# Optimization experiments

Measured on AMD Instinct MI355X. Metric: run time of the kernel, lower is better.

The kernel has to match this reference:

```python
import jax, jax.numpy as jnp
import numpy as np

D_MODEL = 512
N_HEADS = 8
D_HEAD = D_MODEL // N_HEADS
N_LAYERS = 6
VOCAB = 32000
B, S = 4, 1024
EPS = 1e-5


def positional_encoding(length, d_model):
    # matches get_positional_encoding_table: pos * (1/10000**(i/d)), sin on even i, cos on odd i
    inv = 1.0 / (10000.0 ** (jnp.arange(d_model, dtype=jnp.float32) / d_model))
    ang = jnp.arange(length, dtype=jnp.float32)[:, None] * inv[None, :]  # [S, D]
    pe = jnp.where(jnp.arange(d_model) % 2 == 0, jnp.sin(ang), jnp.cos(ang))
    return pe


def layer_norm(x, g, b):
    m = jnp.mean(x, axis=-1, keepdims=True)
    v = jnp.mean((x - m) ** 2, axis=-1, keepdims=True)
    return (x - m) * jax.lax.rsqrt(v + EPS) * g + b


def setup_inputs() -> dict:
    key = jax.random.key(0)
    ks = jax.random.split(key, 9)
    sc = 0.02
    return {
        "tokens": jax.random.randint(ks[0], (B, S), 0, VOCAB),
        "emb": jax.random.normal(ks[1], (VOCAB, D_MODEL), jnp.float32) * sc,
        "Wq": jax.random.normal(ks[2], (N_LAYERS, D_MODEL, D_MODEL), jnp.float32) * sc,
        "bq": jnp.zeros((N_LAYERS, D_MODEL), jnp.float32),
        "Wk": jax.random.normal(ks[3], (N_LAYERS, D_MODEL, D_MODEL), jnp.float32) * sc,
        "bk": jnp.zeros((N_LAYERS, D_MODEL), jnp.float32),
        "Wv": jax.random.normal(ks[4], (N_LAYERS, D_MODEL, D_MODEL), jnp.float32) * sc,
        "bv": jnp.zeros((N_LAYERS, D_MODEL), jnp.float32),
        "Wo": jax.random.normal(ks[5], (N_LAYERS, D_MODEL, D_MODEL), jnp.float32) * sc,
        "bo": jnp.zeros((N_LAYERS, D_MODEL), jnp.float32),
        "W1": jax.random.normal(ks[6], (N_LAYERS, D_MODEL, 4 * D_MODEL), jnp.float32) * sc,
        "b1": jnp.zeros((N_LAYERS, 4 * D_MODEL), jnp.float32),
        "W2": jax.random.normal(ks[7], (N_LAYERS, 4 * D_MODEL, D_MODEL), jnp.float32) * sc,
        "b2": jnp.zeros((N_LAYERS, D_MODEL), jnp.float32),
        "ln_g": jnp.ones((N_LAYERS, D_MODEL), jnp.float32),
        "ln_b": jnp.zeros((N_LAYERS, D_MODEL), jnp.float32),
    }


def encoder_layer(x, Wq, bq, Wk, bk, Wv, bv, Wo, bo, W1, b1, W2, b2, g, b):
    bsz = x.shape[0]
    q = (x @ Wq + bq).reshape(bsz, -1, N_HEADS, D_HEAD).transpose(0, 2, 1, 3)  # [B,h,S,dk]
    k = (x @ Wk + bk).reshape(bsz, -1, N_HEADS, D_HEAD).transpose(0, 2, 1, 3)
    v = (x @ Wv + bv).reshape(bsz, -1, N_HEADS, D_HEAD).transpose(0, 2, 1, 3)
    scores = jnp.einsum('bhqd,bhkd->bhqk', q, k) / (D_HEAD ** 0.5)
    w = jax.nn.softmax(scores, axis=-1)
    attn = jnp.einsum('bhqk,bhkd->bhqd', w, v)  # [B,h,S,dv]
    # faithful to source bug: .view(B,-1,h*dv) WITHOUT transposing heads back
    attn = attn.reshape(bsz, -1, N_HEADS * D_HEAD)  # [B,S,D] with heads/seq interleaved
    x = layer_norm(x + (attn @ Wo + bo), g, b)
    ffn = jnp.maximum(x @ W1 + b1, 0.0) @ W2 + b2
    x = layer_norm(x + ffn, g, b)  # same (shared) LayerNorm params, as in source
    return x


def reference(tokens, emb, Wq, bq, Wk, bk, Wv, bv, Wo, bo, W1, b1, W2, b2, ln_g, ln_b):
    x = emb[tokens]  # [B,S,D]
    x = x + positional_encoding(x.shape[1], D_MODEL)
    for i in range(N_LAYERS):
        x = encoder_layer(x, Wq[i], bq[i], Wk[i], bk[i], Wv[i], bv[i], Wo[i], bo[i],
                          W1[i], b1[i], W2[i], b2[i], ln_g[i], ln_b[i])
    return x
```

## Files before the change

kernel.cpp:

```cpp
#include <hip/hip_runtime.h>
#include <hip/hip_bf16.h>
#include <math.h>

typedef unsigned short ushort_t;
typedef __attribute__((ext_vector_type(8))) short bfrag_t;
typedef __attribute__((ext_vector_type(4))) float facc_t;

#define D_MODEL 512
#define NH 8
#define DH 64
#define NL 6
#define BB 4
#define SS 1024
#define ROWS (BB*SS)
#define DFF 2048

__device__ inline ushort_t f2bf(float f) {
    __hip_bfloat16 h = __float2bfloat16(f);
    return *(ushort_t*)&h;
}
__device__ inline void gload_lds16(const void* g, void* l) {
    __builtin_amdgcn_global_load_lds((const __attribute__((address_space(1))) unsigned int*)g,
                                     (__attribute__((address_space(3))) unsigned int*)l, 16, 0, 0);
}

__global__ __launch_bounds__(256) void embed_pe(const int* __restrict__ tok,
                                                const float* __restrict__ emb,
                                                float* __restrict__ x,
                                                ushort_t* __restrict__ xbf) {
    int row = blockIdx.x;
    int s = row & (SS - 1);
    int t = tok[row];
    const float* e = emb + (size_t)t * D_MODEL;
    for (int i = threadIdx.x; i < D_MODEL; i += 256) {
        float freq = __expf(-9.210340371976184f * ((float)i / (float)D_MODEL));
        float ang = (float)s * freq;
        float pe = (i & 1) ? cosf(ang) : sinf(ang);
        float v = e[i] + pe;
        x[(size_t)row * D_MODEL + i] = v;
        xbf[(size_t)row * D_MODEL + i] = f2bf(v);
    }
}

__global__ __launch_bounds__(256) void prep_weights(const float* __restrict__ Wq,
                                                    const float* __restrict__ Wk,
                                                    const float* __restrict__ Wv,
                                                    const float* __restrict__ Wo,
                                                    const float* __restrict__ W1,
                                                    const float* __restrict__ W2,
                                                    int layer, ushort_t* __restrict__ wlay) {
    __shared__ float tile[32][33];
    int z = blockIdx.z;
    const float* src; ushort_t* dst; int K, N;
    size_t o512 = (size_t)layer * 512 * 512;
    size_t o1M  = (size_t)layer * 512 * 2048;
    switch (z) {
        case 0: src = Wq + o512; dst = wlay;               K = 512;  N = 512;  break;
        case 1: src = Wk + o512; dst = wlay + 262144;      K = 512;  N = 512;  break;
        case 2: src = Wv + o512; dst = wlay + 524288;      K = 512;  N = 512;  break;
        case 3: src = Wo + o512; dst = wlay + 786432;      K = 512;  N = 512;  break;
        case 4: src = W1 + o1M;  dst = wlay + 1048576;     K = 512;  N = 2048; break;
        default:src = W2 + o1M;  dst = wlay + 2097152;     K = 2048; N = 512;  break;
    }
    int n0 = blockIdx.x * 32, k0 = blockIdx.y * 32;
    if (n0 >= N || k0 >= K) return;
    int tx = threadIdx.x & 31, ty = threadIdx.x >> 5;
    #pragma unroll
    for (int i = 0; i < 4; i++)
        tile[ty + i * 8][tx] = src[(size_t)(k0 + ty + i * 8) * N + n0 + tx];
    __syncthreads();
    #pragma unroll
    for (int i = 0; i < 4; i++)
        dst[(size_t)(n0 + ty + i * 8) * K + k0 + tx] = f2bf(tile[tx][ty + i * 8]);
}

__global__ __launch_bounds__(256) void concat_bias(const float* __restrict__ bq,
                                                   const float* __restrict__ bk,
                                                   const float* __restrict__ bv,
                                                   float* __restrict__ bqkv) {
    int l = blockIdx.x;
    for (int i = threadIdx.x; i < 1536; i += 256) {
        float v = (i < 512) ? bq[l * 512 + i]
                : (i < 1024) ? bk[l * 512 + i - 512]
                : bv[l * 512 + i - 1024];
        bqkv[l * 1536 + i] = v;
    }
}

__global__ __launch_bounds__(256) void gemm_mfma(const ushort_t* __restrict__ A,
                                                 const ushort_t* __restrict__ Bt,
                                                 const float* __restrict__ bias,
                                                 float* __restrict__ Cf,
                                                 ushort_t* __restrict__ Cb,
                                                 int N, int K, int relu) {
    __shared__ ushort_t lA[128 * 64];
    __shared__ ushort_t lB[128 * 64];

    const int tid = threadIdx.x;
    const int w = tid >> 6, lane = tid & 63;
    const int wr = w & 1, wc = w >> 1;
    const int lane16 = lane & 15, quad = lane >> 4;
    const int row0 = blockIdx.y * 128, col0 = blockIdx.x * 128;

    facc_t acc[4][4];
    #pragma unroll
    for (int i = 0; i < 4; i++)
        #pragma unroll
        for (int j = 0; j < 4; j++)
            acc[i][j] = (facc_t){0.f, 0.f, 0.f, 0.f};

    for (int k0 = 0; k0 < K; k0 += 64) {
        __syncthreads();
        #pragma unroll
        for (int i = 0; i < 4; i++) {
            int g = w * 256 + i * 64 + lane;
            int r = g >> 3, p = g & 7;
            int q = p ^ (r & 7);
            gload_lds16(A + (size_t)(row0 + r) * K + k0 + q * 8, lA + (size_t)g * 8);
            gload_lds16(Bt + (size_t)(col0 + r) * K + k0 + q * 8, lB + (size_t)g * 8);
        }
        __syncthreads();

        #pragma unroll
        for (int kk = 0; kk < 2; kk++) {
            bfrag_t af[4], bfg[4];
            #pragma unroll
            for (int t = 0; t < 4; t++) {
                int m = wr * 64 + t * 16 + lane16;
                int q = kk * 4 + quad;
                af[t] = *(const bfrag_t*)(lA + ((size_t)m * 8 + (q ^ (m & 7))) * 8);
                int n = wc * 64 + t * 16 + lane16;
                bfg[t] = *(const bfrag_t*)(lB + ((size_t)n * 8 + (q ^ (n & 7))) * 8);
            }
            #pragma unroll
            for (int ti = 0; ti < 4; ti++)
                #pragma unroll
                for (int tj = 0; tj < 4; tj++)
                    acc[ti][tj] = __builtin_amdgcn_mfma_f32_16x16x32_bf16(
                        af[ti], bfg[tj], acc[ti][tj], 0, 0, 0);
        }
    }

    float bv_[4];
    #pragma unroll
    for (int tj = 0; tj < 4; tj++)
        bv_[tj] = bias[col0 + wc * 64 + tj * 16 + lane16];

    #pragma unroll
    for (int ti = 0; ti < 4; ti++) {
        int grow_base = row0 + wr * 64 + ti * 16 + quad * 4;
        #pragma unroll
        for (int tj = 0; tj < 4; tj++) {
            int gcol = col0 + wc * 64 + tj * 16 + lane16;
            #pragma unroll
            for (int rr = 0; rr < 4; rr++) {
                float v = acc[ti][tj][rr] + bv_[tj];
                if (relu) v = fmaxf(v, 0.f);
                size_t idx = (size_t)(grow_base + rr) * N + gcol;
                if (Cf) Cf[idx] = v;
                if (Cb) Cb[idx] = f2bf(v);
            }
        }
    }
}

__global__ __launch_bounds__(256) void gemm_mfma64(const ushort_t* __restrict__ A,
                                                   const ushort_t* __restrict__ Bt,
                                                   const float* __restrict__ bias,
                                                   float* __restrict__ Cf,
                                                   ushort_t* __restrict__ Cb,
                                                   int N, int K, int relu) {
    __shared__ ushort_t lA[64 * 64];
    __shared__ ushort_t lB[64 * 64];

    const int tid = threadIdx.x;
    const int w = tid >> 6, lane = tid & 63;
    const int wr = w & 1, wc = w >> 1;
    const int lane16 = lane & 15, quad = lane >> 4;
    const int row0 = blockIdx.y * 64, col0 = blockIdx.x * 64;

    facc_t acc[2][2];
    #pragma unroll
    for (int i = 0; i < 2; i++)
        #pragma unroll
        for (int j = 0; j < 2; j++)
            acc[i][j] = (facc_t){0.f, 0.f, 0.f, 0.f};

    for (int k0 = 0; k0 < K; k0 += 64) {
        __syncthreads();
        #pragma unroll
        for (int i = 0; i < 2; i++) {
            int g = w * 128 + i * 64 + lane;
            int r = g >> 3, p = g & 7;
            int q = p ^ (r & 7);
            gload_lds16(A + (size_t)(row0 + r) * K + k0 + q * 8, lA + (size_t)g * 8);
            gload_lds16(Bt + (size_t)(col0 + r) * K + k0 + q * 8, lB + (size_t)g * 8);
        }
        __syncthreads();

        #pragma unroll
        for (int kk = 0; kk < 2; kk++) {
            bfrag_t af[2], bfg[2];
            #pragma unroll
            for (int t = 0; t < 2; t++) {
                int m = wr * 32 + t * 16 + lane16;
                int q = kk * 4 + quad;
                af[t] = *(const bfrag_t*)(lA + ((size_t)m * 8 + (q ^ (m & 7))) * 8);
                int n = wc * 32 + t * 16 + lane16;
                bfg[t] = *(const bfrag_t*)(lB + ((size_t)n * 8 + (q ^ (n & 7))) * 8);
            }
            #pragma unroll
            for (int ti = 0; ti < 2; ti++)
                #pragma unroll
                for (int tj = 0; tj < 2; tj++)
                    acc[ti][tj] = __builtin_amdgcn_mfma_f32_16x16x32_bf16(
                        af[ti], bfg[tj], acc[ti][tj], 0, 0, 0);
        }
    }

    float bv_[2];
    #pragma unroll
    for (int tj = 0; tj < 2; tj++)
        bv_[tj] = bias[col0 + wc * 32 + tj * 16 + lane16];

    #pragma unroll
    for (int ti = 0; ti < 2; ti++) {
        int grow_base = row0 + wr * 32 + ti * 16 + quad * 4;
        #pragma unroll
        for (int tj = 0; tj < 2; tj++) {
            int gcol = col0 + wc * 32 + tj * 16 + lane16;
            #pragma unroll
            for (int rr = 0; rr < 4; rr++) {
                float v = acc[ti][tj][rr] + bv_[tj];
                if (relu) v = fmaxf(v, 0.f);
                size_t idx = (size_t)(grow_base + rr) * N + gcol;
                if (Cf) Cf[idx] = v;
                if (Cb) Cb[idx] = f2bf(v);
            }
        }
    }
}

__global__ __launch_bounds__(128) void attn_mfma(const ushort_t* __restrict__ qkv,
                                                 ushort_t* __restrict__ ab) {
    __shared__ __align__(16) ushort_t lK[4096];
    __shared__ __align__(16) ushort_t lVT[4096];
    __shared__ __align__(16) ushort_t lP[2048];

    const int tid = threadIdx.x;
    const int w = tid >> 6, lane = tid & 63;
    const int lane16 = lane & 15, quad = lane >> 4;
    const int qt = blockIdx.x, h = blockIdx.y, b = blockIdx.z;

    const ushort_t* Qrow = qkv + (size_t)(b * SS + qt * 32 + w * 16 + lane16) * 1536 + h * 64;
    bfrag_t qa[2];
    #pragma unroll
    for (int ks = 0; ks < 2; ks++)
        qa[ks] = *(const bfrag_t*)(Qrow + ks * 32 + quad * 8);

    facc_t O[4];
    #pragma unroll
    for (int t = 0; t < 4; t++) O[t] = (facc_t){0.f, 0.f, 0.f, 0.f};
    float mrow[4] = {-INFINITY, -INFINITY, -INFINITY, -INFINITY};
    float lrow[4] = {0.f, 0.f, 0.f, 0.f};

    const int vkey = tid & 63;
    const int vdg  = tid >> 6;

    for (int kt = 0; kt < 16; kt++) {
        #pragma unroll
        for (int i = 0; i < 4; i++) {
            int g = i * 128 + tid;
            int r = g >> 3, p = g & 7;
            int q = p ^ (r & 7);
            gload_lds16(qkv + (size_t)(b * SS + kt * 64 + r) * 1536 + h * 64 + 512 + q * 8,
                        lK + (size_t)g * 8);
        }
        {
            const ushort_t* vsrc = qkv + (size_t)(b * SS + kt * 64 + vkey) * 1536
                                   + h * 64 + 1024 + vdg * 32;
            ushort_t vs[32];
            #pragma unroll
            for (int i4 = 0; i4 < 4; i4++)
                *(uint4*)(vs + i4 * 8) = *(const uint4*)(vsrc + i4 * 8);
            int k8 = vkey >> 3, j = vkey & 7;
            #pragma unroll
            for (int e = 0; e < 32; e++) {
                int n = vdg * 32 + e;
                lVT[(size_t)(n * 8 + (k8 ^ (n & 7))) * 8 + j] = vs[e];
            }
        }
        __syncthreads();

        facc_t sf[4];
        #pragma unroll
        for (int t = 0; t < 4; t++) sf[t] = (facc_t){0.f, 0.f, 0.f, 0.f};
        #pragma unroll
        for (int ks = 0; ks < 2; ks++) {
            #pragma unroll
            for (int t = 0; t < 4; t++) {
                int row = t * 16 + lane16;
                int q = ks * 4 + quad;
                bfrag_t kf = *(const bfrag_t*)(lK + ((size_t)row * 8 + (q ^ (row & 7))) * 8);
                sf[t] = __builtin_amdgcn_mfma_f32_16x16x32_bf16(qa[ks], kf, sf[t], 0, 0, 0);
            }
        }

        float mt_[4], al[4], ps[4];
        #pragma unroll
        for (int r = 0; r < 4; r++)
            mt_[r] = fmaxf(fmaxf(sf[0][r], sf[1][r]), fmaxf(sf[2][r], sf[3][r])) * 0.125f;
        #pragma unroll
        for (int off = 1; off < 16; off <<= 1)
            #pragma unroll
            for (int r = 0; r < 4; r++)
                mt_[r] = fmaxf(mt_[r], __shfl_xor(mt_[r], off));
        #pragma unroll
        for (int r = 0; r < 4; r++) {
            float mn = fmaxf(mrow[r], mt_[r]);
            al[r] = __expf(mrow[r] - mn);
            mrow[r] = mn;
            ps[r] = 0.f;
        }

        ushort_t* Pw = lP + w * 1024;
        #pragma unroll
        for (int t = 0; t < 4; t++) {
            int k8 = t * 2 + (lane16 >> 3);
            int j = lane16 & 7;
            #pragma unroll
            for (int r = 0; r < 4; r++) {
                float p = __expf(sf[t][r] * 0.125f - mrow[r]);
                ps[r] += p;
                int row = quad * 4 + r;
                Pw[(size_t)(row * 8 + (k8 ^ (row & 7))) * 8 + j] = f2bf(p);
            }
        }
        #pragma unroll
        for (int off = 1; off < 16; off <<= 1)
            #pragma unroll
            for (int r = 0; r < 4; r++)
                ps[r] += __shfl_xor(ps[r], off);
        #pragma unroll
        for (int r = 0; r < 4; r++)
            lrow[r] = lrow[r] * al[r] + ps[r];
        #pragma unroll
        for (int t = 0; t < 4; t++)
            #pragma unroll
            for (int r = 0; r < 4; r++)
                O[t][r] *= al[r];

        #pragma unroll
        for (int ks = 0; ks < 2; ks++) {
            int q = ks * 4 + quad;
            bfrag_t pf = *(const bfrag_t*)(Pw + ((size_t)lane16 * 8 + (q ^ (lane16 & 7))) * 8);
            #pragma unroll
            for (int t = 0; t < 4; t++) {
                int n = t * 16 + lane16;
                bfrag_t vf = *(const bfrag_t*)(lVT + ((size_t)n * 8 + (q ^ (n & 7))) * 8);
                O[t] = __builtin_amdgcn_mfma_f32_16x16x32_bf16(pf, vf, O[t], 0, 0, 0);
            }
        }
        __syncthreads();
    }

    size_t obase = ((size_t)((b * NH + h) * SS) + qt * 32 + w * 16 + quad * 4) * DH;
    #pragma unroll
    for (int r = 0; r < 4; r++) {
        float inv = 1.f / lrow[r];
        #pragma unroll
        for (int t = 0; t < 4; t++)
            ab[obase + (size_t)r * DH + t * 16 + lane16] = f2bf(O[t][r] * inv);
    }
}

__global__ __launch_bounds__(256) void add_ln(const float* __restrict__ x,
                                              const float* __restrict__ delta,
                                              const float* __restrict__ g,
                                              const float* __restrict__ bparm,
                                              float* __restrict__ outf,
                                              ushort_t* __restrict__ outb) {
    __shared__ float red[2][4];
    int row = blockIdx.x;
    int t = threadIdx.x;
    const float* xr = x + (size_t)row * D_MODEL;
    const float* dr = delta + (size_t)row * D_MODEL;
    float v0 = xr[t] + dr[t];
    float v1 = xr[t + 256] + dr[t + 256];
    float s = v0 + v1;
    float ss = v0 * v0 + v1 * v1;
    #pragma unroll
    for (int off = 1; off < 64; off <<= 1) {
        s  += __shfl_xor(s, off);
        ss += __shfl_xor(ss, off);
    }
    int lane = t & 63, wid = t >> 6;
    if (lane == 0) { red[0][wid] = s; red[1][wid] = ss; }
    __syncthreads();
    s  = red[0][0] + red[0][1] + red[0][2] + red[0][3];
    ss = red[1][0] + red[1][1] + red[1][2] + red[1][3];
    float mean = s * (1.f / D_MODEL);
    float var = ss * (1.f / D_MODEL) - mean * mean;
    float rinv = rsqrtf(var + 1e-5f);
    float o0 = (v0 - mean) * rinv * g[t]       + bparm[t];
    float o1 = (v1 - mean) * rinv * g[t + 256] + bparm[t + 256];
    float* orow = outf + (size_t)row * D_MODEL;
    orow[t] = o0; orow[t + 256] = o1;
    ushort_t* brow = outb + (size_t)row * D_MODEL;
    brow[t] = f2bf(o0); brow[t + 256] = f2bf(o1);
}

extern "C" void kernel_launch(void* const* d_in, const int* in_sizes, int n_in,
                              void* d_out, int out_size, void* d_ws, size_t ws_size,
                              hipStream_t stream) {
    const int* tokens = (const int*)d_in[0];
    const float* emb = (const float*)d_in[1];
    const float* Wq = (const float*)d_in[2];  const float* bq = (const float*)d_in[3];
    const float* Wk = (const float*)d_in[4];  const float* bk = (const float*)d_in[5];
    const float* Wv = (const float*)d_in[6];  const float* bv = (const float*)d_in[7];
    const float* Wo = (const float*)d_in[8];  const float* bo = (const float*)d_in[9];
    const float* W1 = (const float*)d_in[10]; const float* b1 = (const float*)d_in[11];
    const float* W2 = (const float*)d_in[12]; const float* b2 = (const float*)d_in[13];
    const float* lng = (const float*)d_in[14]; const float* lnb = (const float*)d_in[15];

    char* base = (char*)d_ws;
    ushort_t* wlay = (ushort_t*)(base);
    float*    bqkv = (float*)   (base + 6291456);
    float*    x    = (float*)   (base + 6328320);
    ushort_t* xbf  = (ushort_t*)(base + 14716928);
    float*    tmp  = (float*)   (base + 18911232);
    ushort_t* qkv  = (ushort_t*)(base + 27299840);
    ushort_t* ab   = (ushort_t*)(base + 39882752);
    ushort_t* mid  = qkv;

    ushort_t* wqkv_t = wlay;
    ushort_t* wo_t   = wlay + 786432;
    ushort_t* w1_t   = wlay + 1048576;
    ushort_t* w2_t   = wlay + 2097152;

    concat_bias<<<NL, 256, 0, stream>>>(bq, bk, bv, bqkv);
    embed_pe<<<ROWS, 256, 0, stream>>>(tokens, emb, x, xbf);

    for (int l = 0; l < NL; l++) {
        prep_weights<<<dim3(64, 64, 6), 256, 0, stream>>>(Wq, Wk, Wv, Wo, W1, W2, l, wlay);

        gemm_mfma<<<dim3(12, 32), 256, 0, stream>>>(xbf, wqkv_t, bqkv + l * 1536,
                                                    nullptr, qkv, 1536, 512, 0);
        attn_mfma<<<dim3(32, NH, BB), 128, 0, stream>>>(qkv, ab);

        gemm_mfma64<<<dim3(8, 64), 256, 0, stream>>>(ab, wo_t, bo + l * D_MODEL,
                                                     tmp, nullptr, 512, 512, 0);
        add_ln<<<ROWS, 256, 0, stream>>>(x, tmp, lng + l * D_MODEL, lnb + l * D_MODEL,
                                         x, xbf);

        gemm_mfma<<<dim3(16, 32), 256, 0, stream>>>(xbf, w1_t, b1 + l * DFF,
                                                    nullptr, mid, 2048, 512, 1);
        gemm_mfma64<<<dim3(8, 64), 256, 0, stream>>>(mid, w2_t, b2 + l * D_MODEL,
                                                     tmp, nullptr, 512, 2048, 0);
        float* lnout = (l == NL - 1) ? (float*)d_out : x;
        add_ln<<<ROWS, 256, 0, stream>>>(x, tmp, lng + l * D_MODEL, lnb + l * D_MODEL,
                                         lnout, xbf);
    }
}
```

Before: 965.2 us.

## Double-buffer K/V tiles in attention and use lazy softmax rescaling with exp2

The attention kernel now double-buffers the K and transposed-V shared-memory tiles, so the next tile's global loads are issued before computing on the current one, and it drops one barrier per iteration. The online softmax skips the rescale of the running max, sum and output unless some row's max grows by more than a threshold. Exponentials use exp2 with a prescaled log2e factor. This hides global-load latency and trims ALU work, at the cost of twice the LDS and some extra registers per thread, which can reduce occupancy. Skipping the rescale lets exponentials exceed 1, which is bounded by the threshold.

```diff
diff --git a/kernel.cpp b/kernel.cpp
--- a/kernel.cpp
+++ b/kernel.cpp
@@ -243,8 +243,8 @@
 
 __global__ __launch_bounds__(128) void attn_mfma(const ushort_t* __restrict__ qkv,
                                                  ushort_t* __restrict__ ab) {
-    __shared__ __align__(16) ushort_t lK[4096];
-    __shared__ __align__(16) ushort_t lVT[4096];
+    __shared__ __align__(16) ushort_t lK[2][4096];
+    __shared__ __align__(16) ushort_t lVT[2][4096];
     __shared__ __align__(16) ushort_t lP[2048];
 
     const int tid = threadIdx.x;
@@ -266,31 +266,52 @@
 
     const int vkey = tid & 63;
     const int vdg  = tid >> 6;
-
-    for (int kt = 0; kt < 16; kt++) {
+    const int vk8 = vkey >> 3, vj = vkey & 7;
+
+    const float LOG2E = 1.4426950408889634f;
+    const float SC = 0.125f * 1.4426950408889634f;
+
+    auto stageK = [&](int kt, int buf) {
         #pragma unroll
         for (int i = 0; i < 4; i++) {
             int g = i * 128 + tid;
             int r = g >> 3, p = g & 7;
             int q = p ^ (r & 7);
             gload_lds16(qkv + (size_t)(b * SS + kt * 64 + r) * 1536 + h * 64 + 512 + q * 8,
-                        lK + (size_t)g * 8);
-        }
-        {
-            const ushort_t* vsrc = qkv + (size_t)(b * SS + kt * 64 + vkey) * 1536
-                                   + h * 64 + 1024 + vdg * 32;
-            ushort_t vs[32];
-            #pragma unroll
-            for (int i4 = 0; i4 < 4; i4++)
-                *(uint4*)(vs + i4 * 8) = *(const uint4*)(vsrc + i4 * 8);
-            int k8 = vkey >> 3, j = vkey & 7;
-            #pragma unroll
-            for (int e = 0; e < 32; e++) {
-                int n = vdg * 32 + e;
-                lVT[(size_t)(n * 8 + (k8 ^ (n & 7))) * 8 + j] = vs[e];
-            }
-        }
-        __syncthreads();
+                        &lK[buf][(size_t)g * 8]);
+        }
+    };
+    auto loadV = [&](int kt, ushort_t* vs) {
+        const ushort_t* vsrc = qkv + (size_t)(b * SS + kt * 64 + vkey) * 1536
+                               + h * 64 + 1024 + vdg * 32;
+        #pragma unroll
+        for (int i4 = 0; i4 < 4; i4++)
+            *(uint4*)(vs + i4 * 8) = *(const uint4*)(vsrc + i4 * 8);
+    };
+    auto writeV = [&](const ushort_t* vs, int buf) {
+        #pragma unroll
+        for (int e = 0; e < 32; e++) {
+            int n = vdg * 32 + e;
+            lVT[buf][(size_t)(n * 8 + (vk8 ^ (n & 7))) * 8 + vj] = vs[e];
+        }
+    };
+
+    {
+        ushort_t v0[32];
+        stageK(0, 0);
+        loadV(0, v0);
+        writeV(v0, 0);
+    }
+    __syncthreads();
+
+    for (int kt = 0; kt < 16; kt++) {
+        const int cur = kt & 1;
+
+        ushort_t vn[32];
+        if (kt < 15) {
+            stageK(kt + 1, cur ^ 1);
+            loadV(kt + 1, vn);
+        }
 
         facc_t sf[4];
         #pragma unroll
@@ -301,12 +322,12 @@
             for (int t = 0; t < 4; t++) {
                 int row = t * 16 + lane16;
                 int q = ks * 4 + quad;
-                bfrag_t kf = *(const bfrag_t*)(lK + ((size_t)row * 8 + (q ^ (row & 7))) * 8);
+                bfrag_t kf = *(const bfrag_t*)(&lK[cur][((size_t)row * 8 + (q ^ (row & 7))) * 8]);
                 sf[t] = __builtin_amdgcn_mfma_f32_16x16x32_bf16(qa[ks], kf, sf[t], 0, 0, 0);
             }
         }
 
-        float mt_[4], al[4], ps[4];
+        float mt_[4];
         #pragma unroll
         for (int r = 0; r < 4; r++)
             mt_[r] = fmaxf(fmaxf(sf[0][r], sf[1][r]), fmaxf(sf[2][r], sf[3][r])) * 0.125f;
@@ -315,14 +336,24 @@
             #pragma unroll
             for (int r = 0; r < 4; r++)
                 mt_[r] = fmaxf(mt_[r], __shfl_xor(mt_[r], off));
-        #pragma unroll
-        for (int r = 0; r < 4; r++) {
-            float mn = fmaxf(mrow[r], mt_[r]);
-            al[r] = __expf(mrow[r] - mn);
-            mrow[r] = mn;
-            ps[r] = 0.f;
-        }
-
+
+        bool small = (mt_[0] <= mrow[0] + 8.f) && (mt_[1] <= mrow[1] + 8.f)
+                  && (mt_[2] <= mrow[2] + 8.f) && (mt_[3] <= mrow[3] + 8.f);
+        if (!__all(small)) {
+            #pragma unroll
+            for (int r = 0; r < 4; r++) {
+                float mn = fmaxf(mrow[r], mt_[r]);
+                float al = __builtin_amdgcn_exp2f((mrow[r] - mn) * LOG2E);
+                mrow[r] = mn;
+                lrow[r] *= al;
+                O[0][r] *= al; O[1][r] *= al; O[2][r] *= al; O[3][r] *= al;
+            }
+        }
+        float mC[4];
+        #pragma unroll
+        for (int r = 0; r < 4; r++) mC[r] = mrow[r] * LOG2E;
+
+        float ps[4] = {0.f, 0.f, 0.f, 0.f};
         ushort_t* Pw = lP + w * 1024;
         #pragma unroll
         for (int t = 0; t < 4; t++) {
@@ -330,7 +361,7 @@
             int j = lane16 & 7;
             #pragma unroll
             for (int r = 0; r < 4; r++) {
-                float p = __expf(sf[t][r] * 0.125f - mrow[r]);
+                float p = __builtin_amdgcn_exp2f(fmaf(sf[t][r], SC, -mC[r]));
                 ps[r] += p;
                 int row = quad * 4 + r;
                 Pw[(size_t)(row * 8 + (k8 ^ (row & 7))) * 8 + j] = f2bf(p);
@@ -343,12 +374,7 @@
                 ps[r] += __shfl_xor(ps[r], off);
         #pragma unroll
         for (int r = 0; r < 4; r++)
-            lrow[r] = lrow[r] * al[r] + ps[r];
-        #pragma unroll
-        for (int t = 0; t < 4; t++)
-            #pragma unroll
-            for (int r = 0; r < 4; r++)
-                O[t][r] *= al[r];
+            lrow[r] += ps[r];
 
         #pragma unroll
         for (int ks = 0; ks < 2; ks++) {
@@ -357,10 +383,13 @@
             #pragma unroll
             for (int t = 0; t < 4; t++) {
                 int n = t * 16 + lane16;
-                bfrag_t vf = *(const bfrag_t*)(lVT + ((size_t)n * 8 + (q ^ (n & 7))) * 8);
+                bfrag_t vf = *(const bfrag_t*)(&lVT[cur][((size_t)n * 8 + (q ^ (n & 7))) * 8]);
                 O[t] = __builtin_amdgcn_mfma_f32_16x16x32_bf16(pf, vf, O[t], 0, 0, 0);
             }
         }
+
+        if (kt < 15) writeV(vn, cur ^ 1);
+
         __syncthreads();
     }
 
```

Measured after the change: 940.1 us. 2.6% less time.
